# Performance work log

Measured on AMD Instinct MI355X. Metric: run time of the kernel, lower is better.

The kernel has to match this reference:

```python
import jax, jax.numpy as jnp
import numpy as np

HEADS = 12
DIM_HEAD = 64
PATCHES = 196  # tokens_to_attend (space attention)
DIM = 768
BATCH = 8
FRAMES = 16
TOKENS = FRAMES * PATCHES + 1  # + CLS


def setup_inputs() -> dict:
    key = jax.random.key(0)
    k1, k2, k3 = jax.random.split(key, 3)
    x = jax.random.normal(k1, (BATCH, TOKENS, DIM), dtype=jnp.float32)
    # small init scale keeps softmax logits in a sane range
    W_qkv = jax.random.normal(k2, (DIM, 3 * HEADS * DIM_HEAD), dtype=jnp.float32) * 0.02
    W_0 = jax.random.normal(k3, (HEADS * DIM_HEAD, DIM), dtype=jnp.float32) * 0.02
    return {"x": x, "W_qkv": W_qkv, "W_0": W_0}


def _mhsa(q, k, v, scale):
    # q: [g,h,i,d], k/v: [g,h,j,d]
    s = jnp.einsum('ghid,ghjd->ghij', q, k) * scale
    a = jax.nn.softmax(s, axis=-1)
    return jnp.einsum('ghij,ghjd->ghid', a, v)


def reference(x, W_qkv, W_0):
    b, t, _ = x.shape
    h, dh, p = HEADS, DIM_HEAD, PATCHES
    scale = dh ** -0.5

    qkv = x @ W_qkv  # [b,t,dh*3*h], flattened in (d, k, h) order per einops pattern
    qkv = qkv.reshape(b, t, dh, 3, h)
    q = jnp.transpose(qkv[:, :, :, 0, :], (0, 3, 1, 2))  # [b,h,t,d]
    k = jnp.transpose(qkv[:, :, :, 1, :], (0, 3, 1, 2))
    v = jnp.transpose(qkv[:, :, :, 2, :], (0, 3, 1, 2))

    # CLS query attends over ALL space-time tokens
    cls_q, q3 = q[:, :, :1], q[:, :, 1:]
    out_cls = _mhsa(cls_q, k, v, scale)  # [b,h,1,d]

    cls_k, k3 = k[:, :, :1], k[:, :, 1:]
    cls_v, v3 = v[:, :, :1], v[:, :, 1:]

    f = (t - 1) // p  # frames

    def space_rearrange(z):  # 'b h (f p) d -> (b f) h p d'
        z = z.reshape(b, h, f, p, dh)
        return jnp.transpose(z, (0, 2, 1, 3, 4)).reshape(b * f, h, p, dh)

    q_sep = space_rearrange(q3)
    k_sep = space_rearrange(k3)
    v_sep = space_rearrange(v3)

    # broadcast CLS key/value to every frame group: 'b ... -> (b tile) ...'
    cls_k = jnp.repeat(cls_k, f, axis=0)  # [b*f,h,1,d]
    cls_v = jnp.repeat(cls_v, f, axis=0)

    kk = jnp.concatenate((cls_k, k_sep), axis=2)  # [b*f,h,p+1,d]
    vv = jnp.concatenate((cls_v, v_sep), axis=2)

    out_sp = _mhsa(q_sep, kk, vv, scale)  # [b*f,h,p,d]

    # merge: '(b f) h p d -> b h (f p) d' (space=True path)
    out_sp = out_sp.reshape(b, f, h, p, dh)
    out_sp = jnp.transpose(out_sp, (0, 2, 1, 3, 4)).reshape(b, h, f * p, dh)

    out = jnp.concatenate((out_cls, out_sp), axis=2)  # [b,h,t,d]
    out = jnp.transpose(out, (0, 2, 1, 3)).reshape(b, t, h * dh)
    return out @ W_0
```

## Files before the change

kernel.cpp:

```cpp
#include <hip/hip_runtime.h>
#include <hip/hip_bf16.h>
#include <cstdint>

typedef unsigned short u16;
typedef uint32_t u32;
typedef __attribute__((ext_vector_type(8))) u16 u16x8;
typedef __attribute__((ext_vector_type(4))) u16 u16x4;
typedef __attribute__((ext_vector_type(8))) __bf16 bf16x8;
typedef __attribute__((ext_vector_type(4))) float f32x4;

#define B_    8
#define T_    3137
#define H_    12
#define F_    16
#define D_    768
#define M1    25096
#define VSTR  3200
#define NSPL  16
#define SPK   208

__device__ __forceinline__ u16 f2bf(float f) {
  unsigned u = __float_as_uint(f);
  return (u16)((u + 0x7FFFu + ((u >> 16) & 1u)) >> 16);
}
__device__ __forceinline__ float b2f(u16 v) {
  return __uint_as_float(((unsigned)v) << 16);
}

#define GLL(g, l) __builtin_amdgcn_global_load_lds( \
    (const __attribute__((address_space(1))) void*)(g), \
    (__attribute__((address_space(3))) void*)(l), 16, 0, 0)

__device__ __forceinline__ void dsr(bf16x8& d, u32 abyte) {
  asm volatile("ds_read_b128 %0, %1" : "=v"(d) : "v"(abyte));
}

#define BARR  __builtin_amdgcn_s_barrier()
#define LGKM0 asm volatile("s_waitcnt lgkmcnt(0)")
#define SCB   __builtin_amdgcn_sched_barrier(0)
#define PRI1  __builtin_amdgcn_s_setprio(1)
#define PRI0  __builtin_amdgcn_s_setprio(0)

__global__ __launch_bounds__(256) void k_cvt_x(const float* __restrict__ x,
                                               u16* __restrict__ xb, int n4) {
  int i = blockIdx.x * 256 + threadIdx.x;
  if (i >= n4) return;
  float4 v = ((const float4*)x)[i];
  u16x4 o = { f2bf(v.x), f2bf(v.y), f2bf(v.z), f2bf(v.w) };
  *(u16x4*)(xb + (size_t)i * 4) = o;
}

__global__ __launch_bounds__(256) void k_transpose(const float* __restrict__ in,
                                                   u16* __restrict__ out,
                                                   int R, int C, int qkvperm) {
  __shared__ float tile[32][33];
  int c0 = blockIdx.x * 32, r0 = blockIdx.y * 32;
  int tx = threadIdx.x, ty = threadIdx.y;
  #pragma unroll
  for (int i = ty; i < 32; i += 8)
    tile[i][tx] = in[(size_t)(r0 + i) * C + c0 + tx];
  __syncthreads();
  #pragma unroll
  for (int i = ty; i < 32; i += 8) {
    int c = c0 + i;
    int orow;
    if (qkvperm) {
      int d = c / 36, rem = c - d * 36;
      int comp = rem / 12, hh = rem - comp * 12;
      orow = comp * 768 + hh * 64 + d;
    } else {
      orow = c;
    }
    out[(size_t)orow * R + r0 + tx] = f2bf(tile[tx][i]);
  }
}

template<int EPI, int NX>
__global__ __launch_bounds__(256, 2) void k_gemm(const u16* __restrict__ A,
                                                 const u16* __restrict__ Bm,
                                                 float* __restrict__ outF,
                                                 u16* __restrict__ Qb,
                                                 u16* __restrict__ Kb,
                                                 u16* __restrict__ Vt) {
  __shared__ u16 lds[32768];
  const int tid = threadIdx.x;
  const int lane = tid & 63;
  const int wid = tid >> 6;
  const int wr = wid >> 1, wc = wid & 1;
  const int li = lane & 15, lg = lane >> 4;

  const int nwg = NX * 197;
  const int q = nwg >> 3, r = nwg & 7;
  const int g = blockIdx.x;
  const int xcd = g & 7, pos = g >> 3;
  const int s = ((xcd < r) ? xcd * (q + 1) : r * (q + 1) + (xcd - r) * q) + pos;
  const int arow0 = (s / NX) * 128;
  const int brow0 = (s % NX) * 128;

  const int srow = wid * 32 + (lane >> 3);
  const int scol = ((lane & 7) ^ (lane >> 3)) * 8;
  const u16* gA = A  + (size_t)(arow0 + srow) * 768 + scol;
  const u16* gB = Bm + (size_t)(brow0 + srow) * 768 + scol;

  const u32 ldsb = (u32)(uintptr_t)(__attribute__((address_space(3))) u16*)(&lds[0]);
  const u32 e0 = (u32)((lg ^ (li & 7)) * 16);
  const u32 e1 = (u32)(((lg + 4) ^ (li & 7)) * 16);
  const u32 aA = ldsb + (u32)(wr * 64 + li) * 128;
  const u32 aB = ldsb + 16384 + (u32)(wc * 64 + li) * 128;

  f32x4 acc[4][4] = {};

#define STAGE(TB, KS) do { const int kb_ = (KS) * 64; \
    _Pragma("unroll") for (int c_ = 0; c_ < 4; ++c_) { \
      GLL(gA + kb_ + c_ * 8 * 768, lds + (TB) * 16384 + wid * 2048 + c_ * 512); \
      GLL(gB + kb_ + c_ * 8 * 768, lds + (TB) * 16384 + 8192 + wid * 2048 + c_ * 512); \
    } \
  } while (0)

#define STEP(CUR, KV) do { \
    { const int ks_ = ((KV) + 1 < 12) ? (KV) + 1 : 11; STAGE((CUR) ^ 1, ks_); } \
    asm volatile("s_waitcnt vmcnt(8)"); \
    BARR; \
    bf16x8 af[4][2], bfr[4][2]; \
    _Pragma("unroll") for (int m = 0; m < 4; ++m) { \
      dsr(af[m][0], aA + (CUR) * 32768 + m * 2048 + e0); \
      dsr(af[m][1], aA + (CUR) * 32768 + m * 2048 + e1); } \
    _Pragma("unroll") for (int n = 0; n < 4; ++n) { \
      dsr(bfr[n][0], aB + (CUR) * 32768 + n * 2048 + e0); \
      dsr(bfr[n][1], aB + (CUR) * 32768 + n * 2048 + e1); } \
    LGKM0; SCB; PRI1; \
    _Pragma("unroll") for (int m = 0; m < 4; ++m) \
    _Pragma("unroll") for (int n = 0; n < 4; ++n) { \
      acc[m][n] = __builtin_amdgcn_mfma_f32_16x16x32_bf16(af[m][0], bfr[n][0], acc[m][n], 0, 0, 0); \
      acc[m][n] = __builtin_amdgcn_mfma_f32_16x16x32_bf16(af[m][1], bfr[n][1], acc[m][n], 0, 0, 0); } \
    PRI0; BARR; \
  } while (0)

  STAGE(0, 0);

  #pragma unroll 1
  for (int kk = 0; kk < 12; kk += 2) {
    STEP(0, kk);
    STEP(1, kk + 1);
  }
#undef STAGE
#undef STEP

  if (EPI == 0) {
    #pragma unroll
    for (int m = 0; m < 4; ++m)
      #pragma unroll
      for (int n = 0; n < 4; ++n) {
        const int colp = brow0 + wc * 64 + n * 16 + li;
        #pragma unroll
        for (int rr = 0; rr < 4; ++rr) {
          const int row = arow0 + wr * 64 + m * 16 + lg * 4 + rr;
          if (row < M1)
            __builtin_nontemporal_store(acc[m][n][rr], outF + (size_t)row * 768 + colp);
        }
      }
  } else {
    const int comp = brow0 / 768;
    const float qsc = (comp == 0) ? 0.125f : 1.0f;
    const int b0r = arow0 / T_;
    const int RB = (b0r + 1) * T_;
    __syncthreads();
    if (comp < 2) {
      u16* tl = &lds[0];
      #pragma unroll
      for (int m = 0; m < 4; ++m)
        #pragma unroll
        for (int n = 0; n < 4; ++n)
          #pragma unroll
          for (int rr = 0; rr < 4; ++rr)
            tl[(wr * 64 + m * 16 + lg * 4 + rr) * 136 + wc * 64 + n * 16 + li] =
                f2bf(acc[m][n][rr] * qsc);
      __syncthreads();
      u16* dst = (comp == 0) ? Qb : Kb;
      const int hh0 = (brow0 - comp * 768) >> 6;
      const int grp = tid >> 4, li2 = tid & 15;
      #pragma unroll
      for (int pass = 0; pass < 16; ++pass) {
        const int idx = pass * 16 + grp;
        const int row = idx >> 1, hl = idx & 1;
        const int rg = arow0 + row;
        if (rg >= M1) continue;
        const int bb = (rg >= RB) ? b0r + 1 : b0r;
        const int tt = rg - bb * T_;
        const size_t bh = (size_t)bb * H_ + hh0 + hl;
        *(u16x4*)(dst + ((bh * T_ + tt) << 6) + li2 * 4) =
            *(const u16x4*)(tl + row * 136 + hl * 64 + li2 * 4);
      }
    } else {
      u16* tl = &lds[0];
      #pragma unroll
      for (int m = 0; m < 4; ++m)
        #pragma unroll
        for (int n = 0; n < 4; ++n)
          #pragma unroll
          for (int rr = 0; rr < 4; ++rr)
            tl[(wr * 64 + m * 16 + lg * 4 + rr) * 130 + wc * 64 + n * 16 + li] =
                f2bf(acc[m][n][rr]);
      __syncthreads();
      const int vcol0 = brow0 - 1536;
      #pragma unroll 1
      for (int cc = 0; cc < 32; ++cc) {
        const int c = wid * 32 + cc;
        const int vcol = vcol0 + c;
        const int hh = vcol >> 6, dd = vcol & 63;
        #pragma unroll
        for (int half = 0; half < 2; ++half) {
          const int tloc = half * 64 + lane;
          const int rg = arow0 + tloc;
          if (rg >= M1) continue;
          const int bb = (rg >= RB) ? b0r + 1 : b0r;
          const int tt = rg - bb * T_;
          Vt[(((size_t)bb * H_ + hh) * 64 + dd) * VSTR + tt] = tl[tloc * 130 + c];
        }
      }
    }
  }
}

__global__ __launch_bounds__(512, 2) void k_attn_sp(const u16* __restrict__ Qb,
                                                    const u16* __restrict__ Kb,
                                                    const u16* __restrict__ Vt,
                                                    u16* __restrict__ AO) {
  __shared__ u16 Ks[224 * 64];
  __shared__ u16 Vs[4 * 64 * 64];
  __shared__ u16 P[8][16 * 232];
  const int bid = blockIdx.x;
  const int h = bid % H_;
  const int f = (bid / H_) % F_;
  const int b = bid / (H_ * F_);
  const int tid = threadIdx.x;
  const int lane = tid & 63, w = tid >> 6;
  const int li = lane & 15, lg = lane >> 4;
  const size_t bh = (size_t)b * H_ + h;
  const u16* Qp = Qb + bh * T_ * 64;
  const u16* Kp = Kb + bh * T_ * 64;
  const u16* Vp = Vt + bh * 64 * VSTR;
  u16* ps = &P[w][0];

  if (w < 7) {
    #pragma unroll
    for (int p = 0; p < 4; ++p) {
      const int c = (w * 4 + p) * 64 + lane;
      const int key = c >> 3, sp = lane & 7;
      const int tok = (key == 0) ? 0 : f * 196 + key;
      GLL(Kp + (size_t)tok * 64 + ((sp ^ (key & 7)) * 8), Ks + c * 8);
    }
  }
  {
    const int d = tid & 63, kg = (tid >> 6) & 3, sh = tid >> 8;
    #pragma unroll
    for (int st = 0; st < 2; ++st) {
      const int stt = sh + st * 2;
      const u16* src = Vp + (size_t)d * VSTR + f * 196 + stt * 64 + kg * 16;
      u16x4 a0 = *(const u16x4*)(src);
      u16x4 a1 = *(const u16x4*)(src + 4);
      u16x4 a2 = *(const u16x4*)(src + 8);
      u16x4 a3 = *(const u16x4*)(src + 12);
      if (stt == 0 && kg == 0) a0[0] = Vp[(size_t)d * VSTR];
      u16* row = Vs + stt * 4096 + d * 64;
      const int s0 = (kg * 2) ^ (d & 7), s1 = (kg * 2 + 1) ^ (d & 7);
      u16x8 w0 = { a0[0], a0[1], a0[2], a0[3], a1[0], a1[1], a1[2], a1[3] };
      u16x8 w1 = { a2[0], a2[1], a2[2], a2[3], a3[0], a3[1], a3[2], a3[3] };
      *(u16x8*)(row + s0 * 8) = w0;
      *(u16x8*)(row + s1 * 8) = w1;
    }
  }
  __syncthreads();

  for (int mt = w; mt < 13; mt += 8) {
    const int pp = mt * 16 + li;
    const int ppc = pp < 196 ? pp : 195;
    const size_t tq = 1 + f * 196 + ppc;
    const bf16x8 qf0 = *(const bf16x8*)(Qp + tq * 64 + lg * 8);
    const bf16x8 qf1 = *(const bf16x8*)(Qp + tq * 64 + 32 + lg * 8);

    f32x4 s[14] = {};
    #pragma unroll
    for (int n = 0; n < 14; ++n) {
      const int key = n * 16 + li;
      const u16* kp = Ks + key * 64;
      const bf16x8 kf0 = *(const bf16x8*)(kp + ((lg ^ (li & 7)) * 8));
      const bf16x8 kf1 = *(const bf16x8*)(kp + (((lg + 4) ^ (li & 7)) * 8));
      s[n] = __builtin_amdgcn_mfma_f32_16x16x32_bf16(qf0, kf0, s[n], 0, 0, 0);
      s[n] = __builtin_amdgcn_mfma_f32_16x16x32_bf16(qf1, kf1, s[n], 0, 0, 0);
    }

    float rsum[4];
    #pragma unroll
    for (int r = 0; r < 4; ++r) {
      float vals[14];
      float mx = -1e30f;
      #pragma unroll
      for (int n = 0; n < 14; ++n) {
        const int key = n * 16 + li;
        vals[n] = (key < 197) ? s[n][r] : -1e30f;
        mx = fmaxf(mx, vals[n]);
      }
      #pragma unroll
      for (int msk = 1; msk < 16; msk <<= 1) mx = fmaxf(mx, __shfl_xor(mx, msk));
      float sum = 0.f;
      #pragma unroll
      for (int n = 0; n < 14; ++n) {
        const int key = n * 16 + li;
        float p = (key < 197) ? __expf(vals[n] - mx) : 0.f;
        sum += p;
        ps[(lg * 4 + r) * 232 + key] = f2bf(p);
      }
      #pragma unroll
      for (int msk = 1; msk < 16; msk <<= 1) sum += __shfl_xor(sum, msk);
      rsum[r] = sum;
    }

    f32x4 o[4] = {};
    #pragma unroll
    for (int ks = 0; ks < 7; ++ks) {
      const bf16x8 pf = *(const bf16x8*)(ps + li * 232 + ks * 32 + lg * 8);
      const int slot = ((ks & 1) * 4 + lg);
      #pragma unroll
      for (int n = 0; n < 4; ++n) {
        const int d = n * 16 + li;
        const bf16x8 vf = *(const bf16x8*)(Vs + (ks >> 1) * 4096 + d * 64 +
                                           ((slot ^ (li & 7)) * 8));
        o[n] = __builtin_amdgcn_mfma_f32_16x16x32_bf16(pf, vf, o[n], 0, 0, 0);
      }
    }

    #pragma unroll
    for (int n = 0; n < 4; ++n)
      #pragma unroll
      for (int r = 0; r < 4; ++r)
        ps[(lg * 4 + r) * 64 + n * 16 + li] = f2bf(o[n][r] / rsum[r]);
    #pragma unroll
    for (int p2 = 0; p2 < 2; ++p2) {
      const int row = p2 * 8 + (lane >> 3);
      const int ch = lane & 7;
      const int ppo = mt * 16 + row;
      if (ppo < 196) {
        const size_t t = 1 + (size_t)f * 196 + ppo;
        *(u16x8*)(AO + ((size_t)b * T_ + t) * 768 + h * 64 + ch * 8) =
            *(const u16x8*)(ps + row * 64 + ch * 8);
      }
    }
  }
}

__global__ __launch_bounds__(256) void k_attn_cls1(const u16* __restrict__ Qb,
                                                   const u16* __restrict__ Kb,
                                                   const u16* __restrict__ Vt,
                                                   float* __restrict__ Pc) {
  __shared__ float qs[64];
  __shared__ float sv[SPK];
  __shared__ float red[8];
  const int bid = blockIdx.x;
  const int s = bid & (NSPL - 1);
  const int bh = bid >> 4;
  const u16* Qp = Qb + (size_t)bh * T_ * 64;
  const u16* Kp = Kb + (size_t)bh * T_ * 64;
  const u16* Vp = Vt + (size_t)bh * 64 * VSTR;
  const int base = s * SPK;
  const int nk0 = T_ - base;
  const int nk = (nk0 < SPK) ? nk0 : SPK;
  const int tid = threadIdx.x;
  const int lane = tid & 63, w = tid >> 6;

  if (tid < 64) qs[tid] = b2f(Qp[tid]);
  for (int jj = nk + tid; jj < SPK; jj += 256) sv[jj] = 0.f;
  __syncthreads();

  float lmax = -1e30f;
  for (int jj = tid; jj < nk; jj += 256) {
    const u16* kp = Kp + (size_t)(base + jj) * 64;
    float acc = 0.f;
    #pragma unroll
    for (int d0 = 0; d0 < 64; d0 += 8) {
      u16x8 kv = *(const u16x8*)(kp + d0);
      #pragma unroll
      for (int e = 0; e < 8; ++e) acc += qs[d0 + e] * b2f(kv[e]);
    }
    sv[jj] = acc;
    lmax = fmaxf(lmax, acc);
  }
  #pragma unroll
  for (int msk = 32; msk; msk >>= 1) lmax = fmaxf(lmax, __shfl_xor(lmax, msk));
  if (lane == 0) red[w] = lmax;
  __syncthreads();
  const float bmax = fmaxf(fmaxf(red[0], red[1]), fmaxf(red[2], red[3]));

  float lsum = 0.f;
  for (int jj = tid; jj < nk; jj += 256) {
    float p = __expf(sv[jj] - bmax);
    sv[jj] = p;
    lsum += p;
  }
  #pragma unroll
  for (int msk = 32; msk; msk >>= 1) lsum += __shfl_xor(lsum, msk);
  if (lane == 0) red[4 + w] = lsum;
  __syncthreads();
  const float bsum = red[4] + red[5] + red[6] + red[7];

  const int d = tid >> 2, q4 = tid & 3;
  const u16* vp = Vp + (size_t)d * VSTR + base + q4 * (SPK / 4);
  const float* sp = &sv[q4 * (SPK / 4)];
  float o = 0.f;
  #pragma unroll
  for (int k4 = 0; k4 < SPK / 4; k4 += 4) {
    u16x4 vv = *(const u16x4*)(vp + k4);
    o += sp[k4]     * b2f(vv[0]) + sp[k4 + 1] * b2f(vv[1])
       + sp[k4 + 2] * b2f(vv[2]) + sp[k4 + 3] * b2f(vv[3]);
  }
  o += __shfl_xor(o, 1);
  o += __shfl_xor(o, 2);

  float* P = Pc + ((size_t)bh * NSPL + s) * 66;
  if (tid == 0) { P[0] = bmax; P[1] = bsum; }
  if (q4 == 0) P[2 + d] = o;
}

__global__ __launch_bounds__(64) void k_attn_cls2(const float* __restrict__ Pc,
                                                  u16* __restrict__ AO) {
  const int bh = blockIdx.x;
  const int d = threadIdx.x;
  const float* P = Pc + (size_t)bh * NSPL * 66;
  float m = -1e30f;
  #pragma unroll
  for (int s = 0; s < NSPL; ++s) m = fmaxf(m, P[s * 66]);
  float l = 0.f, o = 0.f;
  #pragma unroll
  for (int s = 0; s < NSPL; ++s) {
    const float wgt = __expf(P[s * 66] - m);
    l += wgt * P[s * 66 + 1];
    o += wgt * P[s * 66 + 2 + d];
  }
  const int b = bh / H_, h = bh - b * H_;
  AO[(size_t)b * T_ * 768 + h * 64 + d] = f2bf(o / l);
}

extern "C" void kernel_launch(void* const* d_in, const int* in_sizes, int n_in,
                              void* d_out, int out_size, void* d_ws, size_t ws_size,
                              hipStream_t stream) {
  const float* x    = (const float*)d_in[0];
  const float* Wqkv = (const float*)d_in[1];
  const float* W0   = (const float*)d_in[2];
  float* out = (float*)d_out;
  char* ws = (char*)d_ws;

  u16* xb    = (u16*)(ws);
  u16* wqkvT = (u16*)(ws + 38731776);
  u16* w0T   = (u16*)(ws + 42270720);
  u16* Qb    = (u16*)(ws + 43450368);
  u16* Kb    = (u16*)(ws + 81997824);
  u16* Vt    = (u16*)(ws + 120545280);
  u16* AO = xb;
  float* Pc = (float*)wqkvT;

  k_cvt_x<<<dim3(18822), dim3(256), 0, stream>>>(x, xb, (M1 * D_) / 4);
  k_transpose<<<dim3(72, 24), dim3(32, 8), 0, stream>>>(Wqkv, wqkvT, 768, 2304, 1);
  k_transpose<<<dim3(24, 24), dim3(32, 8), 0, stream>>>(W0, w0T, 768, 768, 0);
  k_gemm<1, 18><<<dim3(18 * 197), dim3(256), 0, stream>>>(xb, wqkvT, nullptr, Qb, Kb, Vt);
  k_attn_sp<<<dim3(1536), dim3(512), 0, stream>>>(Qb, Kb, Vt, AO);
  k_attn_cls1<<<dim3(96 * NSPL), dim3(256), 0, stream>>>(Qb, Kb, Vt, Pc);
  k_attn_cls2<<<dim3(96), dim3(64), 0, stream>>>(Pc, AO);
  k_gemm<0, 6><<<dim3(6 * 197), dim3(256), 0, stream>>>(AO, w0T, out, nullptr, nullptr, nullptr);
}
```

Baseline: 276.4 us.

## Interleave softmax exponentials with PV MFMA chunks to shrink P buffer and raise occupancy

The space-attention kernel now computes only the row max up front. It then produces the exponentiated probabilities 32 keys at a time, feeding each chunk straight into the P·V MFMAs through a small per-wave LDS staging buffer, and reduces the row sums at the end. Shared memory drops from a 16x232 to a 16x72 tile per wave, and the launch bounds ask for 4 blocks per CU instead of 2, so more blocks can be resident and the exp work can overlap the matrix ops. The risk is register pressure under the tighter launch bound, which could cause spills, plus extra explicit waitcnt fences on the LDS round trip.

```diff
diff --git a/kernel.cpp b/kernel.cpp
--- a/kernel.cpp
+++ b/kernel.cpp
@@ -222,13 +222,13 @@
   }
 }
 
-__global__ __launch_bounds__(512, 2) void k_attn_sp(const u16* __restrict__ Qb,
+__global__ __launch_bounds__(512, 4) void k_attn_sp(const u16* __restrict__ Qb,
                                                     const u16* __restrict__ Kb,
                                                     const u16* __restrict__ Vt,
                                                     u16* __restrict__ AO) {
   __shared__ u16 Ks[224 * 64];
   __shared__ u16 Vs[4 * 64 * 64];
-  __shared__ u16 P[8][16 * 232];
+  __shared__ u16 P[8][16 * 72];
   const int bid = blockIdx.x;
   const int h = bid % H_;
   const int f = (bid / H_) % F_;
@@ -290,36 +290,38 @@
       s[n] = __builtin_amdgcn_mfma_f32_16x16x32_bf16(qf1, kf1, s[n], 0, 0, 0);
     }
 
-    float rsum[4];
+    float mx[4];
     #pragma unroll
     for (int r = 0; r < 4; ++r) {
-      float vals[14];
-      float mx = -1e30f;
+      float m0 = -1e30f;
       #pragma unroll
       for (int n = 0; n < 14; ++n) {
         const int key = n * 16 + li;
-        vals[n] = (key < 197) ? s[n][r] : -1e30f;
-        mx = fmaxf(mx, vals[n]);
-      }
-      #pragma unroll
-      for (int msk = 1; msk < 16; msk <<= 1) mx = fmaxf(mx, __shfl_xor(mx, msk));
-      float sum = 0.f;
-      #pragma unroll
-      for (int n = 0; n < 14; ++n) {
+        m0 = fmaxf(m0, (key < 197) ? s[n][r] : -1e30f);
+      }
+      #pragma unroll
+      for (int msk = 1; msk < 16; msk <<= 1) m0 = fmaxf(m0, __shfl_xor(m0, msk));
+      mx[r] = m0;
+    }
+
+    float rsum[4] = {0.f, 0.f, 0.f, 0.f};
+    f32x4 o[4] = {};
+    #pragma unroll
+    for (int ks = 0; ks < 7; ++ks) {
+      const int cofs = (ks & 1) * 32;
+      #pragma unroll
+      for (int half = 0; half < 2; ++half) {
+        const int n = ks * 2 + half;
         const int key = n * 16 + li;
-        float p = (key < 197) ? __expf(vals[n] - mx) : 0.f;
-        sum += p;
-        ps[(lg * 4 + r) * 232 + key] = f2bf(p);
-      }
-      #pragma unroll
-      for (int msk = 1; msk < 16; msk <<= 1) sum += __shfl_xor(sum, msk);
-      rsum[r] = sum;
-    }
-
-    f32x4 o[4] = {};
-    #pragma unroll
-    for (int ks = 0; ks < 7; ++ks) {
-      const bf16x8 pf = *(const bf16x8*)(ps + li * 232 + ks * 32 + lg * 8);
+        #pragma unroll
+        for (int r = 0; r < 4; ++r) {
+          float p = (key < 197) ? __expf(s[n][r] - mx[r]) : 0.f;
+          rsum[r] += p;
+          ps[(lg * 4 + r) * 72 + cofs + half * 16 + li] = f2bf(p);
+        }
+      }
+      asm volatile("s_waitcnt lgkmcnt(0)" ::: "memory");
+      const bf16x8 pf = *(const bf16x8*)(ps + li * 72 + cofs + lg * 8);
       const int slot = ((ks & 1) * 4 + lg);
       #pragma unroll
       for (int n = 0; n < 4; ++n) {
@@ -331,10 +333,20 @@
     }
 
     #pragma unroll
+    for (int r = 0; r < 4; ++r) {
+      float su = rsum[r];
+      #pragma unroll
+      for (int msk = 1; msk < 16; msk <<= 1) su += __shfl_xor(su, msk);
+      rsum[r] = su;
+    }
+
+    asm volatile("s_waitcnt lgkmcnt(0)" ::: "memory");
+    #pragma unroll
     for (int n = 0; n < 4; ++n)
       #pragma unroll
       for (int r = 0; r < 4; ++r)
         ps[(lg * 4 + r) * 64 + n * 16 + li] = f2bf(o[n][r] / rsum[r]);
+    asm volatile("s_waitcnt lgkmcnt(0)" ::: "memory");
     #pragma unroll
     for (int p2 = 0; p2 < 2; ++p2) {
       const int row = p2 * 8 + (lane >> 3);
```

Measured after the change: 252.9 us, median of 2. -8.5%, faster.
